# Kernel tuning notes

Hardware: AMD Instinct MI355X
Metric: run time of the kernel (lower is better)

## Reference

```python
import jax, jax.numpy as jnp
import numpy as np

D_MODEL = 1024
NUM_HEADS = 16
HEAD_DIM = D_MODEL // NUM_HEADS


def setup_inputs() -> dict:
    key = jax.random.key(0)
    ks = jax.random.split(key, 9)
    s = 1.0 / np.sqrt(D_MODEL)
    def lin(k):
        kw, kb = jax.random.split(k)
        W = jax.random.uniform(kw, (D_MODEL, D_MODEL), jnp.float32, -s, s)
        b = jax.random.uniform(kb, (D_MODEL,), jnp.float32, -s, s)
        return W, b
    Wq, bq = lin(ks[0])
    Wk, bk = lin(ks[1])
    Wv, bv = lin(ks[2])
    Wo, bo = lin(ks[3])
    x = jax.random.normal(ks[4], (4, 2048, D_MODEL), jnp.float32)
    return {"x": x, "Wq": Wq, "bq": bq, "Wk": Wk, "bk": bk,
            "Wv": Wv, "bv": bv, "Wo": Wo, "bo": bo}


def reference(x, Wq, bq, Wk, bk, Wv, bv, Wo, bo):
    B, S, _ = x.shape
    def heads(W, b):
        # [B,S,D] -> [B,H,S,Dh]
        return (x @ W.T + b).reshape(B, S, NUM_HEADS, HEAD_DIM).transpose(0, 2, 1, 3)
    q = heads(Wq, bq)
    k = heads(Wk, bk)
    v = heads(Wv, bv)
    scale = jnp.sqrt(jnp.float32(HEAD_DIM))
    scores = jnp.einsum('bhqd,bhkd->bhqk', q, k) / scale  # [B,H,S,S]
    attn = jax.nn.softmax(scores, axis=-1)
    ctx = jnp.einsum('bhqk,bhkd->bhqd', attn, v)
    ctx = ctx.transpose(0, 2, 1, 3).reshape(B, S, D_MODEL)
    out = ctx @ Wo.T + bo
    return out
```

## Files before the change

kernel.cpp:

```cpp
#include <hip/hip_runtime.h>
#include <hip/hip_bf16.h>

typedef __bf16 bf16;
typedef __attribute__((ext_vector_type(4))) __bf16 bf16x4;
typedef __attribute__((ext_vector_type(8))) __bf16 bf16x8;
typedef __attribute__((ext_vector_type(4))) float floatx4;

#define MFMA_16x16x32(a, b, c) __builtin_amdgcn_mfma_f32_16x16x32_bf16((a), (b), (c), 0, 0, 0)

#define SOFTMAX_SC 0.18033688011112042f

__device__ __forceinline__ void async_lds16(const bf16* g, bf16* lds) {
  __builtin_amdgcn_global_load_lds(
      (__attribute__((address_space(1))) void*)(g),
      (__attribute__((address_space(3))) void*)(lds),
      16, 0, 0);
}

__global__ __launch_bounds__(256) void cast_kernel(const float* __restrict__ src,
                                                   bf16* __restrict__ dst, int n) {
  int i = (blockIdx.x * 256 + threadIdx.x) * 8;
  if (i >= n) return;
  floatx4 a = *(const floatx4*)(src + i);
  floatx4 b = *(const floatx4*)(src + i + 4);
  bf16x8 r;
  r[0] = (bf16)a[0]; r[1] = (bf16)a[1]; r[2] = (bf16)a[2]; r[3] = (bf16)a[3];
  r[4] = (bf16)b[0]; r[5] = (bf16)b[1]; r[6] = (bf16)b[2]; r[7] = (bf16)b[3];
  *(bf16x8*)(dst + i) = r;
}

template <typename CT>
__device__ __forceinline__ void gemm128_async_body(
    const bf16* __restrict__ A, const bf16* __restrict__ W,
    const float* __restrict__ bias, CT* __restrict__ C)
{
  __shared__ __align__(16) bf16 As[128 * 64];
  __shared__ __align__(16) bf16 Bs[128 * 64];

  const int tid  = threadIdx.x;
  const int lane = tid & 63;
  const int wave = tid >> 6;
  const int quad = lane >> 4;
  const int l15  = lane & 15;

  const int gm0   = blockIdx.y * 128;
  const int gn0   = blockIdx.x * 128;
  const int m_off = (wave >> 1) * 64;
  const int n_off = (wave & 1) * 64;

  floatx4 acc[4][4] = {};

  const bf16* ap[4];
  const bf16* wp[4];
  #pragma unroll
  for (int i = 0; i < 4; ++i) {
    int c = i * 256 + tid;
    int srow = c >> 3;
    int ksw  = (c & 7) ^ (srow & 7);
    ap[i] = A + (size_t)(gm0 + srow) * 1024 + ksw * 8;
    wp[i] = W + (size_t)(gn0 + srow) * 1024 + ksw * 8;
  }

  for (int kt = 0; kt < 16; ++kt) {
    __syncthreads();
    #pragma unroll
    for (int i = 0; i < 4; ++i) {
      int c = i * 256 + tid;
      async_lds16(ap[i], &As[c * 8]);
      async_lds16(wp[i], &Bs[c * 8]);
      ap[i] += 64; wp[i] += 64;
    }
    __syncthreads();

    #pragma unroll
    for (int kk = 0; kk < 2; ++kk) {
      bf16x8 af[4], bfr[4];
      #pragma unroll
      for (int i = 0; i < 4; ++i) {
        int rm = m_off + i * 16 + l15;
        af[i]  = *(const bf16x8*)&As[rm * 64 + (((kk * 4 + quad) ^ (rm & 7)) * 8)];
        int rn = n_off + i * 16 + l15;
        bfr[i] = *(const bf16x8*)&Bs[rn * 64 + (((kk * 4 + quad) ^ (rn & 7)) * 8)];
      }
      #pragma unroll
      for (int i = 0; i < 4; ++i)
        #pragma unroll
        for (int j = 0; j < 4; ++j)
          acc[i][j] = MFMA_16x16x32(af[i], bfr[j], acc[i][j]);
    }
  }

  #pragma unroll
  for (int j = 0; j < 4; ++j) {
    const int gcol = gn0 + n_off + j * 16 + l15;
    const float bv = bias[gcol];
    #pragma unroll
    for (int i = 0; i < 4; ++i) {
      const int gr = gm0 + m_off + i * 16 + quad * 4;
      #pragma unroll
      for (int r = 0; r < 4; ++r)
        C[(size_t)(gr + r) * 1024 + gcol] = (CT)(acc[i][j][r] + bv);
    }
  }
}

__global__ __launch_bounds__(256) void o_gemm_async(
    const bf16* __restrict__ ctx, const bf16* __restrict__ Wob,
    const float* __restrict__ bo, float* __restrict__ out)
{
  gemm128_async_body<float>(ctx, Wob, bo, out);
}

__global__ __launch_bounds__(512, 4) void qkv_gemm256(
    const bf16* __restrict__ xb,
    const bf16* __restrict__ Wqb, const float* __restrict__ bq,
    const bf16* __restrict__ Wkb, const float* __restrict__ bk,
    const bf16* __restrict__ Wvb, const float* __restrict__ bv,
    bf16* Q, bf16* K, bf16* Vt)
{
  __shared__ __align__(16) bf16 As[256 * 64];
  __shared__ __align__(16) bf16 Bs[128 * 64];

  const int z = blockIdx.z;
  const bf16* W = (z == 0) ? Wqb : (z == 1) ? Wkb : Wvb;
  const float* bias = (z == 0) ? bq : (z == 1) ? bk : bv;

  const int tid  = threadIdx.x;
  const int lane = tid & 63;
  const int wave = tid >> 6;
  const int quad = lane >> 4;
  const int l15  = lane & 15;

  const int gm0   = blockIdx.y * 256;
  const int gn0   = blockIdx.x * 128;
  const int m_off = (wave >> 1) * 64;
  const int n_off = (wave & 1) * 64;

  floatx4 acc[4][4] = {};

  const bf16* ap[4];
  const bf16* wp[2];
  #pragma unroll
  for (int i = 0; i < 4; ++i) {
    int c = i * 512 + tid;
    int srow = c >> 3;
    int ksw  = (c & 7) ^ (srow & 7);
    ap[i] = xb + (size_t)(gm0 + srow) * 1024 + ksw * 8;
  }
  #pragma unroll
  for (int i = 0; i < 2; ++i) {
    int c = i * 512 + tid;
    int srow = c >> 3;
    int ksw  = (c & 7) ^ (srow & 7);
    wp[i] = W + (size_t)(gn0 + srow) * 1024 + ksw * 8;
  }

  for (int kt = 0; kt < 16; ++kt) {
    __syncthreads();
    #pragma unroll
    for (int i = 0; i < 4; ++i) {
      async_lds16(ap[i], &As[(i * 512 + tid) * 8]);
      ap[i] += 64;
    }
    #pragma unroll
    for (int i = 0; i < 2; ++i) {
      async_lds16(wp[i], &Bs[(i * 512 + tid) * 8]);
      wp[i] += 64;
    }
    __syncthreads();

    #pragma unroll
    for (int kk = 0; kk < 2; ++kk) {
      bf16x8 af[4], bfr[4];
      #pragma unroll
      for (int i = 0; i < 4; ++i) {
        int rm = m_off + i * 16 + l15;
        af[i]  = *(const bf16x8*)&As[rm * 64 + (((kk * 4 + quad) ^ (rm & 7)) * 8)];
        int rn = n_off + i * 16 + l15;
        bfr[i] = *(const bf16x8*)&Bs[rn * 64 + (((kk * 4 + quad) ^ (rn & 7)) * 8)];
      }
      #pragma unroll
      for (int i = 0; i < 4; ++i)
        #pragma unroll
        for (int j = 0; j < 4; ++j)
          acc[i][j] = MFMA_16x16x32(af[i], bfr[j], acc[i][j]);
    }
  }

  #pragma unroll
  for (int j = 0; j < 4; ++j) {
    const int gcol = gn0 + n_off + j * 16 + l15;
    const float bv = bias[gcol];
    #pragma unroll
    for (int i = 0; i < 4; ++i) {
      const int gr = gm0 + m_off + i * 16 + quad * 4;
      if (z == 2) {
        const int h  = gcol >> 6;
        const int dh = gcol & 63;
        const size_t base =
            (((size_t)(gr >> 11) * 16 + h) * 64 + dh) * 2048 + (gr & 2047);
        bf16x4 pk;
        #pragma unroll
        for (int r = 0; r < 4; ++r) pk[r] = (bf16)(acc[i][j][r] + bv);
        *(bf16x4*)&Vt[base] = pk;
      } else {
        bf16* dst = (z == 0) ? Q : K;
        const float sc = (z == 0) ? SOFTMAX_SC : 1.0f;
        #pragma unroll
        for (int r = 0; r < 4; ++r)
          dst[(size_t)(gr + r) * 1024 + gcol] = (bf16)((acc[i][j][r] + bv) * sc);
      }
    }
  }
}

__global__ __launch_bounds__(512) void flash3b_kernel(
    const bf16* __restrict__ Q, const bf16* __restrict__ Kg,
    const bf16* __restrict__ Vtg, bf16* __restrict__ ctx)
{
  __shared__ __align__(16) bf16 Ks[64 * 64];
  __shared__ __align__(16) bf16 Vts[64 * 64];
  __shared__ __align__(16) bf16 Ps[8 * 16 * 72];

  const int tid  = threadIdx.x;
  const int lane = tid & 63;
  const int wave = tid >> 6;
  const int quad = lane >> 4;
  const int l15  = lane & 15;

  const int bh = blockIdx.y;
  const int b  = bh >> 4;
  const int h  = bh & 15;
  const int qt = blockIdx.x;

  const size_t row0 = (size_t)b * 2048;
  const int col0 = h * 64;

  const int qs = qt * 128 + wave * 16 + l15;
  const bf16* qp = Q + (row0 + qs) * 1024 + col0 + quad * 8;
  const bf16x8 qf0 = *(const bf16x8*)(qp);
  const bf16x8 qf1 = *(const bf16x8*)(qp + 32);

  floatx4 o_acc[4] = {};
  float l_part[4] = {0.0f, 0.0f, 0.0f, 0.0f};

  const int srow = tid >> 3;
  const int ksw  = (tid & 7) ^ (srow & 7);
  const bf16* kp = Kg + (row0 + srow) * 1024 + col0 + ksw * 8;
  const bf16* vp = Vtg + ((size_t)bh * 64 + srow) * 2048 + ksw * 8;
  bf16* const ksd = &Ks[tid * 8];
  bf16* const vtd = &Vts[tid * 8];

  for (int kb = 0; kb < 32; ++kb) {
    __syncthreads();
    async_lds16(kp, ksd);
    async_lds16(vp, vtd);
    kp += 64 * 1024;
    vp += 64;
    __syncthreads();

    floatx4 sc[4];
    #pragma unroll
    for (int j = 0; j < 4; ++j) {
      int rk = j * 16 + l15;
      bf16x8 k0 = *(const bf16x8*)&Ks[rk * 64 + ((quad ^ (rk & 7)) * 8)];
      bf16x8 k1 = *(const bf16x8*)&Ks[rk * 64 + (((4 + quad) ^ (rk & 7)) * 8)];
      floatx4 z = {};
      z = MFMA_16x16x32(qf0, k0, z);
      z = MFMA_16x16x32(qf1, k1, z);
      sc[j] = z;
    }

    #pragma unroll
    for (int j = 0; j < 4; ++j)
      #pragma unroll
      for (int r = 0; r < 4; ++r) {
        float p = exp2f(fminf(sc[j][r], 60.0f));
        sc[j][r] = p;
        l_part[r] += p;
      }

    #pragma unroll
    for (int j = 0; j < 4; ++j)
      #pragma unroll
      for (int r = 0; r < 4; ++r)
        Ps[(wave * 16 + quad * 4 + r) * 72 + j * 16 + l15] = (bf16)sc[j][r];

    #pragma unroll
    for (int kk = 0; kk < 2; ++kk) {
      bf16x8 pf = *(const bf16x8*)&Ps[(wave * 16 + l15) * 72 + kk * 32 + quad * 8];
      #pragma unroll
      for (int t = 0; t < 4; ++t) {
        int rd = t * 16 + l15;
        bf16x8 vf = *(const bf16x8*)&Vts[rd * 64 + (((kk * 4 + quad) ^ (rd & 7)) * 8)];
        o_acc[t] = MFMA_16x16x32(pf, vf, o_acc[t]);
      }
    }
  }

  #pragma unroll
  for (int off = 1; off < 16; off <<= 1)
    #pragma unroll
    for (int r = 0; r < 4; ++r)
      l_part[r] += __shfl_xor(l_part[r], off, 64);
  #pragma unroll
  for (int r = 0; r < 4; ++r) l_part[r] = 1.0f / l_part[r];

  #pragma unroll
  for (int t = 0; t < 4; ++t)
    #pragma unroll
    for (int r = 0; r < 4; ++r) {
      int srow2 = qt * 128 + wave * 16 + quad * 4 + r;
      ctx[(row0 + srow2) * 1024 + col0 + t * 16 + l15] = (bf16)(o_acc[t][r] * l_part[r]);
    }
}

__device__ __forceinline__ bf16x8 load8(const bf16* p) { return *(const bf16x8*)p; }
__device__ __forceinline__ bf16x8 load8(const float* p) {
  floatx4 a = *(const floatx4*)p;
  floatx4 b = *(const floatx4*)(p + 4);
  bf16x8 r;
  r[0] = (bf16)a[0]; r[1] = (bf16)a[1]; r[2] = (bf16)a[2]; r[3] = (bf16)a[3];
  r[4] = (bf16)b[0]; r[5] = (bf16)b[1]; r[6] = (bf16)b[2]; r[7] = (bf16)b[3];
  return r;
}

template <typename AT, typename CT>
__device__ __forceinline__ void gemm128_body_fb(
    const AT* __restrict__ A, const float* __restrict__ W,
    const float* __restrict__ bias, CT* __restrict__ C)
{
  constexpr int LDP = 72;
  __shared__ __align__(16) bf16 As[128 * LDP];
  __shared__ __align__(16) bf16 Bs[128 * LDP];
  const int tid = threadIdx.x, lane = tid & 63, wave = tid >> 6;
  const int quad = lane >> 4, l15 = lane & 15;
  const int gm0 = blockIdx.y * 128, gn0 = blockIdx.x * 128;
  const int m_off = (wave >> 1) * 64, n_off = (wave & 1) * 64;
  floatx4 acc[4][4] = {};
  int srow[4], scol[4];
  #pragma unroll
  for (int i = 0; i < 4; ++i) {
    int c = i * 256 + tid;
    srow[i] = c >> 3; scol[i] = (c & 7) * 8;
  }
  for (int kt = 0; kt < 16; ++kt) {
    bf16x8 ar[4], br[4];
    #pragma unroll
    for (int i = 0; i < 4; ++i) {
      ar[i] = load8(A + (size_t)(gm0 + srow[i]) * 1024 + kt * 64 + scol[i]);
      br[i] = load8(W + (size_t)(gn0 + srow[i]) * 1024 + kt * 64 + scol[i]);
    }
    __syncthreads();
    #pragma unroll
    for (int i = 0; i < 4; ++i) {
      *(bf16x8*)&As[srow[i] * LDP + scol[i]] = ar[i];
      *(bf16x8*)&Bs[srow[i] * LDP + scol[i]] = br[i];
    }
    __syncthreads();
    #pragma unroll
    for (int kk = 0; kk < 2; ++kk) {
      bf16x8 af[4], bfr[4];
      #pragma unroll
      for (int i = 0; i < 4; ++i) {
        af[i]  = *(const bf16x8*)&As[(m_off + i * 16 + l15) * LDP + (kk * 4 + quad) * 8];
        bfr[i] = *(const bf16x8*)&Bs[(n_off + i * 16 + l15) * LDP + (kk * 4 + quad) * 8];
      }
      #pragma unroll
      for (int i = 0; i < 4; ++i)
        #pragma unroll
        for (int j = 0; j < 4; ++j)
          acc[i][j] = MFMA_16x16x32(af[i], bfr[j], acc[i][j]);
    }
  }
  #pragma unroll
  for (int j = 0; j < 4; ++j) {
    const int gcol = gn0 + n_off + j * 16 + l15;
    const float bv = bias[gcol];
    #pragma unroll
    for (int i = 0; i < 4; ++i) {
      const int gr = gm0 + m_off + i * 16 + quad * 4;
      #pragma unroll
      for (int r = 0; r < 4; ++r)
        C[(size_t)(gr + r) * 1024 + gcol] = (CT)(acc[i][j][r] + bv);
    }
  }
}

__global__ __launch_bounds__(256) void qkv_gemm_fb(
    const float* __restrict__ x,
    const float* __restrict__ Wq, const float* __restrict__ bq,
    const float* __restrict__ Wk, const float* __restrict__ bk,
    const float* __restrict__ Wv, const float* __restrict__ bv,
    bf16* Q, bf16* K, bf16* V)
{
  const float* W; const float* bias; bf16* out;
  if (blockIdx.z == 0)      { W = Wq; bias = bq; out = Q; }
  else if (blockIdx.z == 1) { W = Wk; bias = bk; out = K; }
  else                      { W = Wv; bias = bv; out = V; }
  gemm128_body_fb<float, bf16>(x, W, bias, out);
}

__global__ __launch_bounds__(256) void out_gemm_fb(
    const bf16* __restrict__ ctx, const float* __restrict__ Wo,
    const float* __restrict__ bo, float* __restrict__ out)
{
  gemm128_body_fb<bf16, float>(ctx, Wo, bo, out);
}

__global__ __launch_bounds__(512) void flash_fb(
    const bf16* Q, const bf16* __restrict__ Kg, const bf16* __restrict__ Vg,
    bf16* ctx)
{
  __shared__ __align__(16) bf16 Ks[64 * 72];
  __shared__ __align__(16) bf16 Vs[64 * 72];
  __shared__ __align__(16) bf16 Vt[64 * 72];
  __shared__ __align__(16) bf16 Ps[8 * 16 * 72];
  const int tid = threadIdx.x, lane = tid & 63, wave = tid >> 6;
  const int quad = lane >> 4, l15 = lane & 15;
  const int bh = blockIdx.y, b = bh >> 4, h = bh & 15, qt = blockIdx.x;
  const size_t row0 = (size_t)b * 2048;
  const int col0 = h * 64;
  const int qs = qt * 128 + wave * 16 + l15;
  const bf16* qp = Q + (row0 + qs) * 1024 + col0 + quad * 8;
  const bf16x8 qf0 = *(const bf16x8*)(qp);
  const bf16x8 qf1 = *(const bf16x8*)(qp + 32);
  floatx4 o_acc[4] = {};
  float l_part[4] = {0.0f, 0.0f, 0.0f, 0.0f};
  const float SC = SOFTMAX_SC;
  const int srow = tid >> 3, scol = (tid & 7) * 8;
  const bf16* kptr = Kg + (row0 + srow) * 1024 + col0 + scol;
  const bf16* vptr = Vg + (row0 + srow) * 1024 + col0 + scol;
  const int td = tid & 63, tg = tid >> 6;
  for (int kb = 0; kb < 32; ++kb) {
    bf16x8 kr = *(const bf16x8*)kptr;
    bf16x8 vr = *(const bf16x8*)vptr;
    kptr += 64 * 1024; vptr += 64 * 1024;
    __syncthreads();
    *(bf16x8*)&Ks[srow * 72 + scol] = kr;
    *(bf16x8*)&Vs[srow * 72 + scol] = vr;
    __syncthreads();
    {
      bf16x8 t;
      #pragma unroll
      for (int j = 0; j < 8; ++j) t[j] = Vs[(tg * 8 + j) * 72 + td];
      *(bf16x8*)&Vt[td * 72 + tg * 8] = t;
    }
    floatx4 sc[4];
    #pragma unroll
    for (int j = 0; j < 4; ++j) {
      int rk = j * 16 + l15;
      bf16x8 k0 = *(const bf16x8*)&Ks[rk * 72 + quad * 8];
      bf16x8 k1 = *(const bf16x8*)&Ks[rk * 72 + 32 + quad * 8];
      floatx4 z = {};
      z = MFMA_16x16x32(qf0, k0, z);
      z = MFMA_16x16x32(qf1, k1, z);
      sc[j] = z;
    }
    #pragma unroll
    for (int j = 0; j < 4; ++j)
      #pragma unroll
      for (int r = 0; r < 4; ++r) {
        float p = exp2f(fminf(sc[j][r] * SC, 60.0f));
        sc[j][r] = p;
        l_part[r] += p;
      }
    #pragma unroll
    for (int j = 0; j < 4; ++j)
      #pragma unroll
      for (int r = 0; r < 4; ++r)
        Ps[(wave * 16 + quad * 4 + r) * 72 + j * 16 + l15] = (bf16)sc[j][r];
    __syncthreads();
    #pragma unroll
    for (int kk = 0; kk < 2; ++kk) {
      bf16x8 pf = *(const bf16x8*)&Ps[(wave * 16 + l15) * 72 + kk * 32 + quad * 8];
      #pragma unroll
      for (int t = 0; t < 4; ++t) {
        bf16x8 vf = *(const bf16x8*)&Vt[(t * 16 + l15) * 72 + kk * 32 + quad * 8];
        o_acc[t] = MFMA_16x16x32(pf, vf, o_acc[t]);
      }
    }
  }
  #pragma unroll
  for (int off = 1; off < 16; off <<= 1)
    #pragma unroll
    for (int r = 0; r < 4; ++r)
      l_part[r] += __shfl_xor(l_part[r], off, 64);
  #pragma unroll
  for (int r = 0; r < 4; ++r) l_part[r] = 1.0f / l_part[r];
  #pragma unroll
  for (int t = 0; t < 4; ++t)
    #pragma unroll
    for (int r = 0; r < 4; ++r) {
      int srow2 = qt * 128 + wave * 16 + quad * 4 + r;
      ctx[(row0 + srow2) * 1024 + col0 + t * 16 + l15] = (bf16)(o_acc[t][r] * l_part[r]);
    }
}

extern "C" void kernel_launch(void* const* d_in, const int* in_sizes, int n_in,
                              void* d_out, int out_size, void* d_ws, size_t ws_size,
                              hipStream_t stream) {
  (void)in_sizes; (void)n_in; (void)out_size;
  const float* x  = (const float*)d_in[0];
  const float* Wq = (const float*)d_in[1];
  const float* bq = (const float*)d_in[2];
  const float* Wk = (const float*)d_in[3];
  const float* bk = (const float*)d_in[4];
  const float* Wv = (const float*)d_in[5];
  const float* bv = (const float*)d_in[6];
  const float* Wo = (const float*)d_in[7];
  const float* bo = (const float*)d_in[8];
  float* out = (float*)d_out;

  const size_t nE = (size_t)8192 * 1024;
  const size_t wE = (size_t)1024 * 1024;
  const size_t need = (5 * nE + 4 * wE) * sizeof(bf16);

  if (ws_size >= need) {
    bf16* Qw   = (bf16*)d_ws;
    bf16* Kw   = Qw + nE;
    bf16* Vtw  = Kw + nE;
    bf16* ctxw = Vtw + nE;
    bf16* xb   = ctxw + nE;
    bf16* Wqb  = xb + nE;
    bf16* Wkb  = Wqb + wE;
    bf16* Wvb  = Wkb + wE;
    bf16* Wob  = Wvb + wE;

    cast_kernel<<<dim3(4096), 256, 0, stream>>>(x, xb, (int)nE);
    cast_kernel<<<dim3(512), 256, 0, stream>>>(Wq, Wqb, (int)wE);
    cast_kernel<<<dim3(512), 256, 0, stream>>>(Wk, Wkb, (int)wE);
    cast_kernel<<<dim3(512), 256, 0, stream>>>(Wv, Wvb, (int)wE);
    cast_kernel<<<dim3(512), 256, 0, stream>>>(Wo, Wob, (int)wE);

    qkv_gemm256<<<dim3(8, 32, 3), 512, 0, stream>>>(
        xb, Wqb, bq, Wkb, bk, Wvb, bv, Qw, Kw, Vtw);
    flash3b_kernel<<<dim3(16, 64), 512, 0, stream>>>(Qw, Kw, Vtw, ctxw);
    o_gemm_async<<<dim3(8, 64), 256, 0, stream>>>(ctxw, Wob, bo, out);
  } else {
    bf16* Qw = (bf16*)d_ws;
    bf16* Kw = Qw + nE;
    bf16* Vw = Kw + nE;
    bf16* ctx = (ws_size >= 4 * nE * sizeof(bf16)) ? (Vw + nE) : Qw;
    qkv_gemm_fb<<<dim3(8, 64, 3), 256, 0, stream>>>(x, Wq, bq, Wk, bk, Wv, bv, Qw, Kw, Vw);
    flash_fb<<<dim3(16, 64), 512, 0, stream>>>(Qw, Kw, Vw, ctx);
    out_gemm_fb<<<dim3(8, 64), 256, 0, stream>>>(ctx, Wo, bo, out);
  }
}
```

Measured before the change: 332.1 us.

## Give each attention wave two query tiles and merge cast launches into one

The flash attention kernel now runs 4 waves of 256 threads, each handling 32 query rows as two 16-row tiles instead of 16. This lets each K and V fragment read from LDS be reused across two MFMA tiles, and softmax exponentiation is fused directly into the score loop. The five separate float-to-bf16 cast launches are merged into one kernel that indexes the contiguous destination workspace. The trade-off is higher register use per wave (launch bounds ask for 4 blocks) and fewer waves per block to hide LDS and global load latency.

```diff
diff --git a/kernel.cpp b/kernel.cpp
--- a/kernel.cpp
+++ b/kernel.cpp
@@ -17,12 +17,25 @@
       16, 0, 0);
 }
 
-__global__ __launch_bounds__(256) void cast_kernel(const float* __restrict__ src,
-                                                   bf16* __restrict__ dst, int n) {
-  int i = (blockIdx.x * 256 + threadIdx.x) * 8;
-  if (i >= n) return;
-  floatx4 a = *(const floatx4*)(src + i);
-  floatx4 b = *(const floatx4*)(src + i + 4);
+__global__ __launch_bounds__(256) void cast_all_kernel(
+    const float* __restrict__ x,
+    const float* __restrict__ Wq, const float* __restrict__ Wk,
+    const float* __restrict__ Wv, const float* __restrict__ Wo,
+    bf16* __restrict__ dst)
+{
+  const size_t xN = (size_t)8192 * 1024;
+  size_t i = ((size_t)blockIdx.x * 256 + threadIdx.x) * 8;
+  const float* src;
+  size_t off;
+  if (i < xN) { src = x; off = i; }
+  else {
+    size_t j = i - xN;
+    int w = (int)(j >> 20);
+    off = j & (((size_t)1 << 20) - 1);
+    src = (w == 0) ? Wq : (w == 1) ? Wk : (w == 2) ? Wv : Wo;
+  }
+  floatx4 a = *(const floatx4*)(src + off);
+  floatx4 b = *(const floatx4*)(src + off + 4);
   bf16x8 r;
   r[0] = (bf16)a[0]; r[1] = (bf16)a[1]; r[2] = (bf16)a[2]; r[3] = (bf16)a[3];
   r[4] = (bf16)b[0]; r[5] = (bf16)b[1]; r[6] = (bf16)b[2]; r[7] = (bf16)b[3];
@@ -214,13 +227,13 @@
   }
 }
 
-__global__ __launch_bounds__(512) void flash3b_kernel(
+__global__ __launch_bounds__(256, 4) void flash5_kernel(
     const bf16* __restrict__ Q, const bf16* __restrict__ Kg,
     const bf16* __restrict__ Vtg, bf16* __restrict__ ctx)
 {
   __shared__ __align__(16) bf16 Ks[64 * 64];
   __shared__ __align__(16) bf16 Vts[64 * 64];
-  __shared__ __align__(16) bf16 Ps[8 * 16 * 72];
+  __shared__ __align__(16) bf16 Ps[4 * 32 * 72];
 
   const int tid  = threadIdx.x;
   const int lane = tid & 63;
@@ -236,83 +249,93 @@
   const size_t row0 = (size_t)b * 2048;
   const int col0 = h * 64;
 
-  const int qs = qt * 128 + wave * 16 + l15;
-  const bf16* qp = Q + (row0 + qs) * 1024 + col0 + quad * 8;
-  const bf16x8 qf0 = *(const bf16x8*)(qp);
-  const bf16x8 qf1 = *(const bf16x8*)(qp + 32);
-
-  floatx4 o_acc[4] = {};
-  float l_part[4] = {0.0f, 0.0f, 0.0f, 0.0f};
-
-  const int srow = tid >> 3;
-  const int ksw  = (tid & 7) ^ (srow & 7);
-  const bf16* kp = Kg + (row0 + srow) * 1024 + col0 + ksw * 8;
-  const bf16* vp = Vtg + ((size_t)bh * 64 + srow) * 2048 + ksw * 8;
-  bf16* const ksd = &Ks[tid * 8];
-  bf16* const vtd = &Vts[tid * 8];
+  const int qbase = qt * 128 + wave * 32;
+  bf16x8 qf[2][2];
+  #pragma unroll
+  for (int q = 0; q < 2; ++q) {
+    const bf16* qp = Q + (row0 + qbase + q * 16 + l15) * 1024 + col0 + quad * 8;
+    qf[q][0] = *(const bf16x8*)(qp);
+    qf[q][1] = *(const bf16x8*)(qp + 32);
+  }
+
+  floatx4 o_acc[2][4] = {};
+  float l_part[2][4] = {};
+
+  const bf16* kp[2]; const bf16* vp[2];
+  #pragma unroll
+  for (int i = 0; i < 2; ++i) {
+    int c = i * 256 + tid;
+    int row = c >> 3;
+    int cell = (c & 7) ^ (row & 7);
+    kp[i] = Kg + (row0 + row) * 1024 + col0 + cell * 8;
+    vp[i] = Vtg + ((size_t)bh * 64 + row) * 2048 + cell * 8;
+  }
 
   for (int kb = 0; kb < 32; ++kb) {
     __syncthreads();
-    async_lds16(kp, ksd);
-    async_lds16(vp, vtd);
-    kp += 64 * 1024;
-    vp += 64;
-    __syncthreads();
-
-    floatx4 sc[4];
+    async_lds16(kp[0], &Ks[tid * 8]);
+    async_lds16(kp[1], &Ks[(256 + tid) * 8]);
+    async_lds16(vp[0], &Vts[tid * 8]);
+    async_lds16(vp[1], &Vts[(256 + tid) * 8]);
+    kp[0] += 64 * 1024; kp[1] += 64 * 1024;
+    vp[0] += 64;        vp[1] += 64;
+    __syncthreads();
+
     #pragma unroll
     for (int j = 0; j < 4; ++j) {
       int rk = j * 16 + l15;
       bf16x8 k0 = *(const bf16x8*)&Ks[rk * 64 + ((quad ^ (rk & 7)) * 8)];
       bf16x8 k1 = *(const bf16x8*)&Ks[rk * 64 + (((4 + quad) ^ (rk & 7)) * 8)];
-      floatx4 z = {};
-      z = MFMA_16x16x32(qf0, k0, z);
-      z = MFMA_16x16x32(qf1, k1, z);
-      sc[j] = z;
-    }
-
-    #pragma unroll
-    for (int j = 0; j < 4; ++j)
-      #pragma unroll
-      for (int r = 0; r < 4; ++r) {
-        float p = exp2f(fminf(sc[j][r], 60.0f));
-        sc[j][r] = p;
-        l_part[r] += p;
-      }
-
-    #pragma unroll
-    for (int j = 0; j < 4; ++j)
-      #pragma unroll
-      for (int r = 0; r < 4; ++r)
-        Ps[(wave * 16 + quad * 4 + r) * 72 + j * 16 + l15] = (bf16)sc[j][r];
+      #pragma unroll
+      for (int q = 0; q < 2; ++q) {
+        floatx4 z = {};
+        z = MFMA_16x16x32(qf[q][0], k0, z);
+        z = MFMA_16x16x32(qf[q][1], k1, z);
+        #pragma unroll
+        for (int r = 0; r < 4; ++r) {
+          float p = exp2f(fminf(z[r], 60.0f));
+          l_part[q][r] += p;
+          Ps[(wave * 32 + q * 16 + quad * 4 + r) * 72 + j * 16 + l15] = (bf16)p;
+        }
+      }
+    }
 
     #pragma unroll
     for (int kk = 0; kk < 2; ++kk) {
-      bf16x8 pf = *(const bf16x8*)&Ps[(wave * 16 + l15) * 72 + kk * 32 + quad * 8];
+      bf16x8 vf[4];
       #pragma unroll
       for (int t = 0; t < 4; ++t) {
         int rd = t * 16 + l15;
-        bf16x8 vf = *(const bf16x8*)&Vts[rd * 64 + (((kk * 4 + quad) ^ (rd & 7)) * 8)];
-        o_acc[t] = MFMA_16x16x32(pf, vf, o_acc[t]);
-      }
-    }
-  }
-
-  #pragma unroll
-  for (int off = 1; off < 16; off <<= 1)
-    #pragma unroll
-    for (int r = 0; r < 4; ++r)
-      l_part[r] += __shfl_xor(l_part[r], off, 64);
-  #pragma unroll
-  for (int r = 0; r < 4; ++r) l_part[r] = 1.0f / l_part[r];
-
-  #pragma unroll
-  for (int t = 0; t < 4; ++t)
-    #pragma unroll
-    for (int r = 0; r < 4; ++r) {
-      int srow2 = qt * 128 + wave * 16 + quad * 4 + r;
-      ctx[(row0 + srow2) * 1024 + col0 + t * 16 + l15] = (bf16)(o_acc[t][r] * l_part[r]);
-    }
+        vf[t] = *(const bf16x8*)&Vts[rd * 64 + (((kk * 4 + quad) ^ (rd & 7)) * 8)];
+      }
+      #pragma unroll
+      for (int q = 0; q < 2; ++q) {
+        bf16x8 pf = *(const bf16x8*)&Ps[(wave * 32 + q * 16 + l15) * 72 + kk * 32 + quad * 8];
+        #pragma unroll
+        for (int t = 0; t < 4; ++t)
+          o_acc[q][t] = MFMA_16x16x32(pf, vf[t], o_acc[q][t]);
+      }
+    }
+  }
+
+  #pragma unroll
+  for (int q = 0; q < 2; ++q) {
+    #pragma unroll
+    for (int off = 1; off < 16; off <<= 1)
+      #pragma unroll
+      for (int r = 0; r < 4; ++r)
+        l_part[q][r] += __shfl_xor(l_part[q][r], off, 64);
+    #pragma unroll
+    for (int r = 0; r < 4; ++r) l_part[q][r] = 1.0f / l_part[q][r];
+    #pragma unroll
+    for (int t = 0; t < 4; ++t)
+      #pragma unroll
+      for (int r = 0; r < 4; ++r) {
+        int srow = qbase + q * 16 + quad * 4 + r;
+        ctx[(row0 + srow) * 1024 + col0 + t * 16 + l15] =
+            (bf16)(o_acc[q][t][r] * l_part[q][r]);
+      }
+  }
 }
 
 __device__ __forceinline__ bf16x8 load8(const bf16* p) { return *(const bf16x8*)p; }
@@ -527,15 +550,11 @@
     bf16* Wvb  = Wkb + wE;
     bf16* Wob  = Wvb + wE;
 
-    cast_kernel<<<dim3(4096), 256, 0, stream>>>(x, xb, (int)nE);
-    cast_kernel<<<dim3(512), 256, 0, stream>>>(Wq, Wqb, (int)wE);
-    cast_kernel<<<dim3(512), 256, 0, stream>>>(Wk, Wkb, (int)wE);
-    cast_kernel<<<dim3(512), 256, 0, stream>>>(Wv, Wvb, (int)wE);
-    cast_kernel<<<dim3(512), 256, 0, stream>>>(Wo, Wob, (int)wE);
+    cast_all_kernel<<<dim3(6144), 256, 0, stream>>>(x, Wq, Wk, Wv, Wo, xb);
 
     qkv_gemm256<<<dim3(8, 32, 3), 512, 0, stream>>>(
         xb, Wqb, bq, Wkb, bk, Wvb, bv, Qw, Kw, Vtw);
-    flash3b_kernel<<<dim3(16, 64), 512, 0, stream>>>(Qw, Kw, Vtw, ctxw);
+    flash5_kernel<<<dim3(16, 64), 256, 0, stream>>>(Qw, Kw, Vtw, ctxw);
     o_gemm_async<<<dim3(8, 64), 256, 0, stream>>>(ctxw, Wob, bo, out);
   } else {
     bf16* Qw = (bf16*)d_ws;
```

Measured after the change: 322.8 us. -2.8%, faster.
